# Optimization experiments

Measured on AMD Instinct MI355X. Metric: run time of the kernel, lower is better.

## Reference

```python
import jax, jax.numpy as jnp
import numpy as np

K = 16            # neighbors
QUERY_CHUNK = 256 # SE is applied per chunk of this many query points (matches torch loop)
EPS = 1e-5        # BatchNorm eps (eval mode, running stats)


def bn(x, g, b, m, v):
    # eval-mode batchnorm over last axis (channel-last layout here)
    return (x - m) * (g / jnp.sqrt(v + EPS)) + b


def setup_inputs() -> dict:
    key = jax.random.key(0)
    ks = jax.random.split(key, 16)
    B, Cin, N = 4, 128, 4096
    H, Cout = 128, 256
    se_h = Cout // 4
    r = lambda k, s, sc=1.0: jax.random.normal(k, s, jnp.float32) * sc
    return dict(
        x=r(ks[0], (B, Cin, N)),
        W_edge=r(ks[1], (H, 2 * Cin), 0.05),          # edge_mlp conv2d 1x1
        bn1_g=jnp.ones((H,), jnp.float32), bn1_b=jnp.zeros((H,), jnp.float32),
        bn1_m=r(ks[2], (H,), 0.1), bn1_v=jax.random.uniform(ks[3], (H,), jnp.float32) + 0.5,
        w_att=r(ks[4], (H,), 0.1),                     # att_conv (1,H,1,1)
        W_fuse=r(ks[5], (Cout, H), 0.05),              # fuse conv1d
        bn2_g=jnp.ones((Cout,), jnp.float32), bn2_b=jnp.zeros((Cout,), jnp.float32),
        bn2_m=r(ks[6], (Cout,), 0.1), bn2_v=jax.random.uniform(ks[7], (Cout,), jnp.float32) + 0.5,
        fc1_w=r(ks[8], (se_h, Cout), 0.05), fc1_b=jnp.zeros((se_h,), jnp.float32),
        fc2_w=r(ks[9], (Cout, se_h), 0.05), fc2_b=jnp.zeros((Cout,), jnp.float32),
        W_res=r(ks[10], (Cout, Cin), 0.05),            # res_conv conv1d (in!=out)
        bn3_g=jnp.ones((Cout,), jnp.float32), bn3_b=jnp.zeros((Cout,), jnp.float32),
        bn3_m=r(ks[11], (Cout,), 0.1), bn3_v=jax.random.uniform(ks[12], (Cout,), jnp.float32) + 0.5,
    )


def reference(x, W_edge, bn1_g, bn1_b, bn1_m, bn1_v, w_att,
              W_fuse, bn2_g, bn2_b, bn2_m, bn2_v,
              fc1_w, fc1_b, fc2_w, fc2_b,
              W_res, bn3_g, bn3_b, bn3_m, bn3_v):
    B, Cin, N = x.shape
    x_t = jnp.swapaxes(x, 1, 2)  # (B,N,Cin)

    # KNN on features (dynamic=False -> knn on x.transpose); squared euclidean
    # has the same ordering as torch.cdist(p=2).
    sq = jnp.sum(x_t * x_t, axis=-1)                               # (B,N)
    d2 = sq[:, :, None] + sq[:, None, :] - 2.0 * jnp.einsum('bnc,bmc->bnm', x_t, x_t)
    _, idx = jax.lax.top_k(-d2, K)                                  # (B,N,K) smallest dists

    neigh = jax.vmap(lambda p, i: p[i])(x_t, idx)                   # (B,N,K,Cin)
    center = jnp.broadcast_to(x_t[:, :, None, :], neigh.shape)      # (B,N,K,Cin)
    edge = jnp.concatenate([neigh - center, center], axis=-1)       # (B,N,K,2Cin)

    # edge_mlp: 1x1 conv + BN + ReLU
    h = jax.nn.relu(bn(jnp.einsum('bnkc,hc->bnkh', edge, W_edge),
                       bn1_g, bn1_b, bn1_m, bn1_v))                 # (B,N,K,H)

    # attention over neighbors
    att = jax.nn.softmax(jnp.einsum('bnkh,h->bnk', h, w_att), axis=-1)
    agg = jnp.einsum('bnkh,bnk->bnh', h, att)                       # (B,N,H)

    # fuse conv1d + BN + ReLU
    out = jax.nn.relu(bn(jnp.einsum('bnh,oh->bno', agg, W_fuse),
                         bn2_g, bn2_b, bn2_m, bn2_v))               # (B,N,Cout)

    # SE channel attention, applied per query chunk (matches torch loop semantics)
    Cout = out.shape[-1]
    nc = N // QUERY_CHUNK
    oc = out.reshape(B, nc, QUERY_CHUNK, Cout)
    s = oc.mean(axis=2)                                             # (B,nc,Cout)
    s = jax.nn.relu(jnp.einsum('bmc,hc->bmh', s, fc1_w) + fc1_b)
    s = jax.nn.sigmoid(jnp.einsum('bmh,ch->bmc', s, fc2_w) + fc2_b)
    out = (oc * s[:, :, None, :]).reshape(B, N, Cout)

    # residual projection (in_channels != out_channels)
    res = bn(jnp.einsum('bnc,oc->bno', x_t, W_res), bn3_g, bn3_b, bn3_m, bn3_v)
    out = out + res
    return jnp.swapaxes(out, 1, 2)                                  # (B,Cout,N)
```

## Files before the change

### kernel.cpp

```cpp
#include <hip/hip_runtime.h>
#include <cstddef>

typedef __bf16 bf16;
typedef __bf16 bf16x8 __attribute__((ext_vector_type(8)));
typedef float  f32x4  __attribute__((ext_vector_type(4)));
typedef unsigned short u16;
typedef unsigned long long u64;

#define MFMA16x16(a, b, c) __builtin_amdgcn_mfma_f32_16x16x32_bf16((a), (b), (c), 0, 0, 0)

namespace {
constexpr int BB   = 4;
constexpr int CIN  = 128;
constexpr int NPT  = 4096;
constexpr int KNBR = 16;
constexpr int HED  = 128;
constexpr int COUT = 256;
}

__device__ __forceinline__ unsigned int ord_f32(float f) {
  unsigned int b = __float_as_uint(f);
  return b ^ (0x80000000u | (unsigned int)((int)b >> 31));
}
__device__ __forceinline__ u64 mk_key(float d, int m) {
  return ((u64)ord_f32(d) << 32) | (unsigned int)m;
}

__device__ __forceinline__ void sort16(u64* k) {
  #pragma unroll
  for (int sz = 2; sz <= 16; sz <<= 1) {
    #pragma unroll
    for (int st = sz >> 1; st > 0; st >>= 1) {
      #pragma unroll
      for (int i = 0; i < 16; ++i) {
        const int j = i ^ st;
        if (j > i) {
          const bool up = ((i & sz) == 0);
          const u64 a = k[i], c = k[j];
          const bool sw = up ? (a > c) : (a < c);
          k[i] = sw ? c : a;
          k[j] = sw ? a : c;
        }
      }
    }
  }
}

__device__ __forceinline__ void merge16(u64* R, const u64* B) {
  u64 t[16];
  #pragma unroll
  for (int i = 0; i < 16; ++i) {
    const u64 a = R[i], c = B[15 - i];
    t[i] = (a < c) ? a : c;
  }
  #pragma unroll
  for (int st = 8; st > 0; st >>= 1) {
    #pragma unroll
    for (int i = 0; i < 16; ++i) {
      const int j = i ^ st;
      if (j > i) {
        const u64 a = t[i], c = t[j];
        const bool sw = a > c;
        t[i] = sw ? c : a;
        t[j] = sw ? a : c;
      }
    }
  }
  #pragma unroll
  for (int i = 0; i < 16; ++i) R[i] = t[i];
}

__device__ __forceinline__ void shfl_merge16(u64* R, int mask) {
  u64 B[16];
  #pragma unroll
  for (int i = 0; i < 16; ++i) B[i] = __shfl_xor(R[i], mask, 64);
  merge16(R, B);
}

__global__ __launch_bounds__(256) void k_wconv(const float* __restrict__ We,
                                               const float* __restrict__ Wf,
                                               const float* __restrict__ Wr,
                                               bf16* __restrict__ Web,
                                               bf16* __restrict__ Wfb,
                                               bf16* __restrict__ Wrb) {
  const int i = blockIdx.x * 256 + threadIdx.x;
  const int a = i >> 15;
  const int j = i & 32767;
  const float* src = (a == 0) ? We : (a == 1) ? Wf : Wr;
  bf16*        dst = (a == 0) ? Web : (a == 1) ? Wfb : Wrb;
  dst[j] = (bf16)src[j];
}

__global__ __launch_bounds__(256) void k_prep(const float* __restrict__ x,
                                              bf16* __restrict__ xh,
                                              bf16* __restrict__ xl,
                                              float* __restrict__ sq) {
  __shared__ __attribute__((aligned(16))) bf16 th[64][136];
  __shared__ __attribute__((aligned(16))) bf16 tl[64][136];
  __shared__ float sqp[4][64];
  const int tid = threadIdx.x;
  const int b   = blockIdx.x >> 6;
  const int n0  = (blockIdx.x & 63) << 6;
  const int nl  = tid & 63;
  const int cg  = tid >> 6;
  const float* xb = x + (size_t)b * CIN * NPT;
  float acc = 0.f;
  #pragma unroll
  for (int rep = 0; rep < 32; ++rep) {
    const int c = rep * 4 + cg;
    const float v = xb[(size_t)c * NPT + n0 + nl];
    const bf16 h = (bf16)v;
    const bf16 l = (bf16)(v - (float)h);
    acc += v * v;
    th[nl][c] = h;
    tl[nl][c] = l;
  }
  sqp[cg][nl] = acc;
  __syncthreads();
  bf16* xho = xh + ((size_t)b * NPT + n0) * CIN;
  bf16* xlo = xl + ((size_t)b * NPT + n0) * CIN;
  #pragma unroll
  for (int rep = 0; rep < 32; ++rep) {
    const int e = rep * 256 + tid;
    const int r = e >> 7;
    const int c = e & 127;
    xho[(size_t)r * CIN + c] = th[r][c];
    xlo[(size_t)r * CIN + c] = tl[r][c];
  }
  if (tid < 64) {
    sq[b * NPT + n0 + tid] = sqp[0][tid] + sqp[1][tid] + sqp[2][tid] + sqp[3][tid];
  }
}

__global__ __launch_bounds__(256, 2) void k_knn(const bf16* __restrict__ xh,
                                                const bf16* __restrict__ xl,
                                                const float* __restrict__ sq,
                                                int* __restrict__ knn_idx) {
  __shared__ u64 Lk[32][66];
  const int tid  = threadIdx.x;
  const int w    = tid >> 6;
  const int lane = tid & 63;
  const int col  = lane & 15;
  const int quad = lane >> 4;
  const int b    = blockIdx.x >> 7;
  const int q0   = (blockIdx.x & 127) << 5;
  const bf16*  xhb = xh + (size_t)b * NPT * CIN;
  const bf16*  xlb = xl + (size_t)b * NPT * CIN;
  const float* sqb = sq + b * NPT;

  bf16x8 qh[2][4], ql[2][4];
  float sqn[2];
  #pragma unroll
  for (int t = 0; t < 2; ++t) {
    const bf16* qrh = xhb + (size_t)(q0 + t * 16 + col) * CIN + quad * 8;
    const bf16* qrl = xlb + (size_t)(q0 + t * 16 + col) * CIN + quad * 8;
    #pragma unroll
    for (int ks = 0; ks < 4; ++ks) {
      qh[t][ks] = *(const bf16x8*)(qrh + ks * 32);
      ql[t][ks] = *(const bf16x8*)(qrl + ks * 32);
    }
    sqn[t] = sqb[q0 + t * 16 + col];
  }

  u64 R0[16], R1[16];
  #pragma unroll
  for (int i = 0; i < 16; ++i) { R0[i] = ~0ull; R1[i] = ~0ull; }

  const int cbase = w << 10;
  for (int mt = 0; mt < 16; ++mt) {
    const int m0 = cbase + (mt << 6);
    u64 k0[16], k1[16];
    #pragma unroll
    for (int cb = 0; cb < 4; ++cb) {
      const bf16* crh = xhb + (size_t)(m0 + cb * 16 + col) * CIN + quad * 8;
      const bf16* crl = xlb + (size_t)(m0 + cb * 16 + col) * CIN + quad * 8;
      f32x4 a0 = {0.f, 0.f, 0.f, 0.f};
      f32x4 a1 = {0.f, 0.f, 0.f, 0.f};
      #pragma unroll
      for (int ks = 0; ks < 4; ++ks) {
        const bf16x8 ch_ = *(const bf16x8*)(crh + ks * 32);
        const bf16x8 cl_ = *(const bf16x8*)(crl + ks * 32);
        a0 = MFMA16x16(cl_, qh[0][ks], a0);
        a0 = MFMA16x16(ch_, ql[0][ks], a0);
        a0 = MFMA16x16(ch_, qh[0][ks], a0);
        a1 = MFMA16x16(cl_, qh[1][ks], a1);
        a1 = MFMA16x16(ch_, ql[1][ks], a1);
        a1 = MFMA16x16(ch_, qh[1][ks], a1);
      }
      const f32x4 sqm = *(const f32x4*)(sqb + m0 + cb * 16 + quad * 4);
      #pragma unroll
      for (int r = 0; r < 4; ++r) {
        const int m = m0 + cb * 16 + quad * 4 + r;
        k0[cb * 4 + r] = mk_key((sqn[0] + sqm[r]) - 2.0f * a0[r], m);
        k1[cb * 4 + r] = mk_key((sqn[1] + sqm[r]) - 2.0f * a1[r], m);
      }
    }
    sort16(k0); merge16(R0, k0);
    sort16(k1); merge16(R1, k1);
  }

  shfl_merge16(R0, 16);
  shfl_merge16(R0, 32);
  shfl_merge16(R1, 16);
  shfl_merge16(R1, 32);

  if (quad == 0) {
    #pragma unroll
    for (int i = 0; i < 16; ++i) {
      Lk[col][w * 16 + i]        = R0[i];
      Lk[16 | col][w * 16 + i]   = R1[i];
    }
  }
  __syncthreads();

  if (tid < 64) {
    const int q = tid >> 1;
    const int j = tid & 1;
    u64 A[16], Bv[16];
    #pragma unroll
    for (int i = 0; i < 16; ++i) {
      A[i]  = Lk[q][(2 * j) * 16 + i];
      Bv[i] = Lk[q][(2 * j + 1) * 16 + i];
    }
    merge16(A, Bv);
    #pragma unroll
    for (int i = 0; i < 16; ++i) Lk[q][j * 16 + i] = A[i];
  }
  __syncthreads();
  if (tid < 32) {
    u64 A[16], Bv[16];
    #pragma unroll
    for (int i = 0; i < 16; ++i) {
      A[i]  = Lk[tid][i];
      Bv[i] = Lk[tid][16 + i];
    }
    merge16(A, Bv);
    int* op = knn_idx + (size_t)(b * NPT + q0 + tid) * KNBR;
    #pragma unroll
    for (int i = 0; i < 16; ++i) op[i] = (int)(A[i] & 0xFFFFFFFFull);
  }
}

__global__ __launch_bounds__(256) void k_edge(const bf16* __restrict__ xh,
                                              const bf16* __restrict__ xl,
                                              const int* __restrict__ knn_idx,
                                              const bf16* __restrict__ We,
                                              const float* __restrict__ g1, const float* __restrict__ b1,
                                              const float* __restrict__ m1, const float* __restrict__ v1,
                                              const float* __restrict__ watt,
                                              bf16* __restrict__ agg) {
  __shared__ __attribute__((aligned(16))) bf16 Ew[4][16][264];
  __shared__ float s1[HED], t1[HED], wat[HED];
  const int tid  = threadIdx.x;
  const int w    = tid >> 6;
  const int lane = tid & 63;
  const int col  = lane & 15;
  const int quad = lane >> 4;
  if (tid < HED) {
    const float ss = g1[tid] / sqrtf(v1[tid] + 1e-5f);
    s1[tid] = ss;
    t1[tid] = b1[tid] - m1[tid] * ss;
    wat[tid] = watt[tid];
  }
  __syncthreads();
  const int gw = blockIdx.x * 4 + w;
  for (int it = 0; it < 4; ++it) {
    const int p = gw * 4 + it;
    const int b = p >> 12;
    const int n = p & 4095;
    const bf16* xhb = xh + (size_t)b * NPT * CIN;
    const bf16* xlb = xl + (size_t)b * NPT * CIN;
    const int my = knn_idx[(size_t)p * KNBR + col];
    const int m  = __shfl(my, lane >> 2);
    const int sub = lane & 3;
    const int kn  = lane >> 2;
    const bf16* nh = xhb + (size_t)m * CIN + sub * 32;
    const bf16* nl_ = xlb + (size_t)m * CIN + sub * 32;
    const bf16* ch = xhb + (size_t)n * CIN + sub * 32;
    const bf16* cl = xlb + (size_t)n * CIN + sub * 32;
    #pragma unroll
    for (int j = 0; j < 4; ++j) {
      const bf16x8 nhv = *(const bf16x8*)(nh + j * 8);
      const bf16x8 nlv = *(const bf16x8*)(nl_ + j * 8);
      const bf16x8 chv = *(const bf16x8*)(ch + j * 8);
      const bf16x8 clv = *(const bf16x8*)(cl + j * 8);
      bf16x8 dv, cv;
      #pragma unroll
      for (int e = 0; e < 8; ++e) {
        const float nf = (float)nhv[e] + (float)nlv[e];
        const float cf = (float)chv[e] + (float)clv[e];
        dv[e] = (bf16)(nf - cf);
        cv[e] = (bf16)cf;
      }
      *(bf16x8*)&Ew[w][kn][sub * 32 + j * 8]       = dv;
      *(bf16x8*)&Ew[w][kn][128 + sub * 32 + j * 8] = cv;
    }
    __syncthreads();
    const f32x4 zero4 = {0.f, 0.f, 0.f, 0.f};
    f32x4 acc[8];
    #pragma unroll
    for (int hb = 0; hb < 8; ++hb) acc[hb] = zero4;
    #pragma unroll
    for (int ks = 0; ks < 8; ++ks) {
      const bf16x8 af = *(const bf16x8*)&Ew[w][col][ks * 32 + quad * 8];
      #pragma unroll
      for (int hb = 0; hb < 8; ++hb) {
        const bf16x8 bfv = *(const bf16x8*)(We + (size_t)(hb * 16 + col) * 256 + ks * 32 + quad * 8);
        acc[hb] = MFMA16x16(af, bfv, acc[hb]);
      }
    }
    float h[8][4];
    float lg[4] = {0.f, 0.f, 0.f, 0.f};
    #pragma unroll
    for (int hb = 0; hb < 8; ++hb) {
      const int hc = hb * 16 + col;
      const float ss = s1[hc], tt = t1[hc], ww = wat[hc];
      #pragma unroll
      for (int r = 0; r < 4; ++r) {
        const float hv = fmaxf(acc[hb][r] * ss + tt, 0.f);
        h[hb][r] = hv;
        lg[r] += hv * ww;
      }
    }
    #pragma unroll
    for (int r = 0; r < 4; ++r) {
      float vv = lg[r];
      vv += __shfl_xor(vv, 1);
      vv += __shfl_xor(vv, 2);
      vv += __shfl_xor(vv, 4);
      vv += __shfl_xor(vv, 8);
      lg[r] = vv;
    }
    float mx = fmaxf(fmaxf(lg[0], lg[1]), fmaxf(lg[2], lg[3]));
    mx = fmaxf(mx, __shfl_xor(mx, 16));
    mx = fmaxf(mx, __shfl_xor(mx, 32));
    float ex[4];
    float sm = 0.f;
    #pragma unroll
    for (int r = 0; r < 4; ++r) { ex[r] = expf(lg[r] - mx); sm += ex[r]; }
    sm += __shfl_xor(sm, 16);
    sm += __shfl_xor(sm, 32);
    const float inv = 1.0f / sm;
    float ag[8];
    #pragma unroll
    for (int hb = 0; hb < 8; ++hb) {
      float a = h[hb][0] * ex[0] + h[hb][1] * ex[1] + h[hb][2] * ex[2] + h[hb][3] * ex[3];
      a += __shfl_xor(a, 16);
      a += __shfl_xor(a, 32);
      ag[hb] = a * inv;
    }
    if (quad == 0) {
      bf16* ao = agg + (size_t)p * HED;
      #pragma unroll
      for (int hb = 0; hb < 8; ++hb) ao[hb * 16 + col] = (bf16)ag[hb];
    }
    __syncthreads();
  }
}

__global__ __launch_bounds__(256) void k_fuse(const bf16* __restrict__ agg,
                                              const bf16* __restrict__ Wf,
                                              const float* __restrict__ g2, const float* __restrict__ b2,
                                              const float* __restrict__ m2, const float* __restrict__ v2,
                                              bf16* __restrict__ outp) {
  const int tid  = threadIdx.x;
  const int w    = tid >> 6;
  const int lane = tid & 63;
  const int col  = lane & 15;
  const int quad = lane >> 4;
  const int p0   = (blockIdx.x * 4 + w) * 16;
  bf16x8 afr[4];
  const bf16* arow = agg + (size_t)(p0 + col) * HED + quad * 8;
  #pragma unroll
  for (int ks = 0; ks < 4; ++ks) afr[ks] = *(const bf16x8*)(arow + ks * 32);
  #pragma unroll
  for (int ob = 0; ob < 16; ++ob) {
    f32x4 acc = {0.f, 0.f, 0.f, 0.f};
    const bf16* brow = Wf + (size_t)(ob * 16 + col) * HED + quad * 8;
    #pragma unroll
    for (int ks = 0; ks < 4; ++ks)
      acc = MFMA16x16(afr[ks], *(const bf16x8*)(brow + ks * 32), acc);
    const int o = ob * 16 + col;
    const float ss = g2[o] / sqrtf(v2[o] + 1e-5f);
    const float tt = b2[o] - m2[o] * ss;
    #pragma unroll
    for (int r = 0; r < 4; ++r) {
      outp[(size_t)(p0 + quad * 4 + r) * COUT + o] = (bf16)fmaxf(acc[r] * ss + tt, 0.f);
    }
  }
}

__global__ __launch_bounds__(256) void k_se(const bf16* __restrict__ outp,
                                            const float* __restrict__ f1w, const float* __restrict__ f1b,
                                            const float* __restrict__ f2w, const float* __restrict__ f2b,
                                            float* __restrict__ sse) {
  __shared__ float mean_s[COUT];
  __shared__ float h1[64];
  const int bc  = blockIdx.x;
  const int tid = threadIdx.x;
  const bf16* base = outp + (size_t)bc * 256 * COUT;
  float s = 0.f;
  for (int p2 = 0; p2 < 256; ++p2) s += (float)base[(size_t)p2 * COUT + tid];
  mean_s[tid] = s * (1.0f / 256.0f);
  __syncthreads();
  if (tid < 64) {
    float a = f1b[tid];
    for (int c = 0; c < COUT; ++c) a += f1w[tid * COUT + c] * mean_s[c];
    h1[tid] = fmaxf(a, 0.f);
  }
  __syncthreads();
  float a = f2b[tid];
  #pragma unroll
  for (int j = 0; j < 64; ++j) a += f2w[tid * 64 + j] * h1[j];
  sse[(size_t)bc * COUT + tid] = 1.0f / (1.0f + expf(-a));
}

__global__ __launch_bounds__(256) void k_final(const bf16* __restrict__ xh,
                                               const bf16* __restrict__ Wr,
                                               const float* __restrict__ g3, const float* __restrict__ b3,
                                               const float* __restrict__ m3, const float* __restrict__ v3,
                                               const bf16* __restrict__ outp,
                                               const float* __restrict__ sse,
                                               float* __restrict__ out) {
  const int tid  = threadIdx.x;
  const int w    = tid >> 6;
  const int lane = tid & 63;
  const int col  = lane & 15;
  const int quad = lane >> 4;
  const int p0   = (blockIdx.x * 4 + w) * 16;
  const int b    = p0 >> 12;
  const int n0l  = p0 & 4095;
  bf16x8 afr[4];
  const bf16* arow = xh + (size_t)(p0 + col) * CIN + quad * 8;
  #pragma unroll
  for (int ks = 0; ks < 4; ++ks) afr[ks] = *(const bf16x8*)(arow + ks * 32);
  const float* scb = sse + (size_t)(b * 16 + (n0l >> 8)) * COUT;
  #pragma unroll
  for (int ob = 0; ob < 16; ++ob) {
    f32x4 acc = {0.f, 0.f, 0.f, 0.f};
    const bf16* brow = Wr + (size_t)(ob * 16 + col) * CIN + quad * 8;
    #pragma unroll
    for (int ks = 0; ks < 4; ++ks)
      acc = MFMA16x16(afr[ks], *(const bf16x8*)(brow + ks * 32), acc);
    const int o = ob * 16 + col;
    const float ss = g3[o] / sqrtf(v3[o] + 1e-5f);
    const float tt = b3[o] - m3[o] * ss;
    const float sc = scb[o];
    f32x4 pk;
    #pragma unroll
    for (int r = 0; r < 4; ++r) {
      const float res = acc[r] * ss + tt;
      pk[r] = (float)outp[(size_t)(p0 + quad * 4 + r) * COUT + o] * sc + res;
    }
    float* op = out + (size_t)(b * COUT + o) * NPT + n0l + quad * 4;
    *(f32x4*)op = pk;
  }
}

extern "C" void kernel_launch(void* const* d_in, const int* in_sizes, int n_in,
                              void* d_out, int out_size, void* d_ws, size_t ws_size,
                              hipStream_t stream) {
  (void)in_sizes; (void)n_in; (void)out_size; (void)ws_size;
  const float* x    = (const float*)d_in[0];
  const float* We   = (const float*)d_in[1];
  const float* g1   = (const float*)d_in[2];
  const float* b1   = (const float*)d_in[3];
  const float* m1   = (const float*)d_in[4];
  const float* v1   = (const float*)d_in[5];
  const float* watt = (const float*)d_in[6];
  const float* Wf   = (const float*)d_in[7];
  const float* g2   = (const float*)d_in[8];
  const float* b2   = (const float*)d_in[9];
  const float* m2   = (const float*)d_in[10];
  const float* v2   = (const float*)d_in[11];
  const float* f1w  = (const float*)d_in[12];
  const float* f1b  = (const float*)d_in[13];
  const float* f2w  = (const float*)d_in[14];
  const float* f2b  = (const float*)d_in[15];
  const float* Wr   = (const float*)d_in[16];
  const float* g3   = (const float*)d_in[17];
  const float* b3   = (const float*)d_in[18];
  const float* m3   = (const float*)d_in[19];
  const float* v3   = (const float*)d_in[20];

  char* ws = (char*)d_ws;
  size_t off = 0;
  bf16*  xth  = (bf16*)(ws + off);  off += (size_t)BB * NPT * CIN * 2;
  bf16*  xtl  = (bf16*)(ws + off);  off += (size_t)BB * NPT * CIN * 2;
  float* sq   = (float*)(ws + off); off += (size_t)BB * NPT * 4;
  int*   idxp = (int*)(ws + off);   off += (size_t)BB * NPT * KNBR * 4;
  bf16*  aggp = (bf16*)(ws + off);  off += (size_t)BB * NPT * HED * 2;
  bf16*  outp = (bf16*)(ws + off);  off += (size_t)BB * NPT * COUT * 2;
  float* ssep = (float*)(ws + off); off += (size_t)BB * 16 * COUT * 4;
  bf16*  Web  = (bf16*)(ws + off);  off += (size_t)HED * 2 * CIN * 2;
  bf16*  Wfb  = (bf16*)(ws + off);  off += (size_t)COUT * HED * 2;
  bf16*  Wrb  = (bf16*)(ws + off);  off += (size_t)COUT * CIN * 2;

  float* out = (float*)d_out;

  k_wconv<<<384, 256, 0, stream>>>(We, Wf, Wr, Web, Wfb, Wrb);
  k_prep<<<256, 256, 0, stream>>>(x, xth, xtl, sq);
  k_knn<<<512, 256, 0, stream>>>(xth, xtl, sq, idxp);
  k_edge<<<1024, 256, 0, stream>>>(xth, xtl, idxp, Web, g1, b1, m1, v1, watt, aggp);
  k_fuse<<<256, 256, 0, stream>>>(aggp, Wfb, g2, b2, m2, v2, outp);
  k_se<<<64, 256, 0, stream>>>(outp, f1w, f1b, f2w, f2b, ssep);
  k_final<<<256, 256, 0, stream>>>(xth, Wrb, g3, b3, m3, v3, outp, ssep, out);
}
```

Before: 434.3 us.

## Two-pass KNN: float-only top-k threshold, then recompute and collect candidates

Measured after the change: 513.5 us. 18.2% more time.

```diff
diff --git a/kernel.cpp b/kernel.cpp
--- a/kernel.cpp
+++ b/kernel.cpp
@@ -70,11 +70,51 @@
   for (int i = 0; i < 16; ++i) R[i] = t[i];
 }
 
-__device__ __forceinline__ void shfl_merge16(u64* R, int mask) {
-  u64 B[16];
+__device__ __forceinline__ void fsort16(float* k) {
+  #pragma unroll
+  for (int sz = 2; sz <= 16; sz <<= 1) {
+    #pragma unroll
+    for (int st = sz >> 1; st > 0; st >>= 1) {
+      #pragma unroll
+      for (int i = 0; i < 16; ++i) {
+        const int j = i ^ st;
+        if (j > i) {
+          const bool up = ((i & sz) == 0);
+          const float a = k[i], c = k[j];
+          const float lo = fminf(a, c), hi = fmaxf(a, c);
+          k[i] = up ? lo : hi;
+          k[j] = up ? hi : lo;
+        }
+      }
+    }
+  }
+}
+
+__device__ __forceinline__ void fmerge16(float* R, const float* B) {
+  float t[16];
+  #pragma unroll
+  for (int i = 0; i < 16; ++i) t[i] = fminf(R[i], B[15 - i]);
+  #pragma unroll
+  for (int st = 8; st > 0; st >>= 1) {
+    #pragma unroll
+    for (int i = 0; i < 16; ++i) {
+      const int j = i ^ st;
+      if (j > i) {
+        const float a = t[i], c = t[j];
+        t[i] = fminf(a, c);
+        t[j] = fmaxf(a, c);
+      }
+    }
+  }
+  #pragma unroll
+  for (int i = 0; i < 16; ++i) R[i] = t[i];
+}
+
+__device__ __forceinline__ void fshfl_merge16(float* R, int mask) {
+  float B[16];
   #pragma unroll
   for (int i = 0; i < 16; ++i) B[i] = __shfl_xor(R[i], mask, 64);
-  merge16(R, B);
+  fmerge16(R, B);
 }
 
 __global__ __launch_bounds__(256) void k_wconv(const float* __restrict__ We,
@@ -136,7 +176,10 @@
                                                 const bf16* __restrict__ xl,
                                                 const float* __restrict__ sq,
                                                 int* __restrict__ knn_idx) {
-  __shared__ u64 Lk[32][66];
+  __shared__ float Lf[32][66];
+  __shared__ float Thr[32];
+  __shared__ unsigned int cnt[32];
+  __shared__ u64 buf[32][32];
   const int tid  = threadIdx.x;
   const int w    = tid >> 6;
   const int lane = tid & 63;
@@ -162,14 +205,18 @@
     sqn[t] = sqb[q0 + t * 16 + col];
   }
 
-  u64 R0[16], R1[16];
-  #pragma unroll
-  for (int i = 0; i < 16; ++i) { R0[i] = ~0ull; R1[i] = ~0ull; }
+  float R0[16], R1[16];
+  #pragma unroll
+  for (int i = 0; i < 16; ++i) {
+    R0[i] = __builtin_inff();
+    R1[i] = __builtin_inff();
+  }
 
   const int cbase = w << 10;
+
   for (int mt = 0; mt < 16; ++mt) {
     const int m0 = cbase + (mt << 6);
-    u64 k0[16], k1[16];
+    float k0v[16], k1v[16];
     #pragma unroll
     for (int cb = 0; cb < 4; ++cb) {
       const bf16* crh = xhb + (size_t)(m0 + cb * 16 + col) * CIN + quad * 8;
@@ -190,25 +237,26 @@
       const f32x4 sqm = *(const f32x4*)(sqb + m0 + cb * 16 + quad * 4);
       #pragma unroll
       for (int r = 0; r < 4; ++r) {
-        const int m = m0 + cb * 16 + quad * 4 + r;
-        k0[cb * 4 + r] = mk_key((sqn[0] + sqm[r]) - 2.0f * a0[r], m);
-        k1[cb * 4 + r] = mk_key((sqn[1] + sqm[r]) - 2.0f * a1[r], m);
-      }
-    }
-    sort16(k0); merge16(R0, k0);
-    sort16(k1); merge16(R1, k1);
-  }
-
-  shfl_merge16(R0, 16);
-  shfl_merge16(R0, 32);
-  shfl_merge16(R1, 16);
-  shfl_merge16(R1, 32);
+        const float s0 = sqn[0] + sqm[r];
+        const float s1 = sqn[1] + sqm[r];
+        k0v[cb * 4 + r] = fmaf(-2.0f, a0[r], s0);
+        k1v[cb * 4 + r] = fmaf(-2.0f, a1[r], s1);
+      }
+    }
+    fsort16(k0v); fmerge16(R0, k0v);
+    fsort16(k1v); fmerge16(R1, k1v);
+  }
+
+  fshfl_merge16(R0, 16);
+  fshfl_merge16(R0, 32);
+  fshfl_merge16(R1, 16);
+  fshfl_merge16(R1, 32);
 
   if (quad == 0) {
     #pragma unroll
     for (int i = 0; i < 16; ++i) {
-      Lk[col][w * 16 + i]        = R0[i];
-      Lk[16 | col][w * 16 + i]   = R1[i];
+      Lf[col][w * 16 + i]      = R0[i];
+      Lf[16 | col][w * 16 + i] = R1[i];
     }
   }
   __syncthreads();
@@ -216,23 +264,98 @@
   if (tid < 64) {
     const int q = tid >> 1;
     const int j = tid & 1;
-    u64 A[16], Bv[16];
+    float A[16], Bv[16];
     #pragma unroll
     for (int i = 0; i < 16; ++i) {
-      A[i]  = Lk[q][(2 * j) * 16 + i];
-      Bv[i] = Lk[q][(2 * j + 1) * 16 + i];
-    }
-    merge16(A, Bv);
-    #pragma unroll
-    for (int i = 0; i < 16; ++i) Lk[q][j * 16 + i] = A[i];
+      A[i]  = Lf[q][(2 * j) * 16 + i];
+      Bv[i] = Lf[q][(2 * j + 1) * 16 + i];
+    }
+    fmerge16(A, Bv);
+    #pragma unroll
+    for (int i = 0; i < 16; ++i) Lf[q][j * 16 + i] = A[i];
+  }
+  __syncthreads();
+  if (tid < 32) {
+    float A[16], Bv[16];
+    #pragma unroll
+    for (int i = 0; i < 16; ++i) {
+      A[i]  = Lf[tid][i];
+      Bv[i] = Lf[tid][16 + i];
+    }
+    fmerge16(A, Bv);
+    Thr[tid] = A[15];
+    cnt[tid] = 0;
+  }
+  __syncthreads();
+
+  const float thr0 = Thr[col];
+  const float thr1 = Thr[16 | col];
+
+  for (int mt = 0; mt < 16; ++mt) {
+    const int m0 = cbase + (mt << 6);
+    #pragma unroll
+    for (int cb = 0; cb < 4; ++cb) {
+      const bf16* crh = xhb + (size_t)(m0 + cb * 16 + col) * CIN + quad * 8;
+      const bf16* crl = xlb + (size_t)(m0 + cb * 16 + col) * CIN + quad * 8;
+      f32x4 a0 = {0.f, 0.f, 0.f, 0.f};
+      f32x4 a1 = {0.f, 0.f, 0.f, 0.f};
+      #pragma unroll
+      for (int ks = 0; ks < 4; ++ks) {
+        const bf16x8 ch_ = *(const bf16x8*)(crh + ks * 32);
+        const bf16x8 cl_ = *(const bf16x8*)(crl + ks * 32);
+        a0 = MFMA16x16(cl_, qh[0][ks], a0);
+        a0 = MFMA16x16(ch_, ql[0][ks], a0);
+        a0 = MFMA16x16(ch_, qh[0][ks], a0);
+        a1 = MFMA16x16(cl_, qh[1][ks], a1);
+        a1 = MFMA16x16(ch_, ql[1][ks], a1);
+        a1 = MFMA16x16(ch_, qh[1][ks], a1);
+      }
+      const f32x4 sqm = *(const f32x4*)(sqb + m0 + cb * 16 + quad * 4);
+      #pragma unroll
+      for (int r = 0; r < 4; ++r) {
+        const int m = m0 + cb * 16 + quad * 4 + r;
+        const float s0 = sqn[0] + sqm[r];
+        const float s1 = sqn[1] + sqm[r];
+        const float d0 = fmaf(-2.0f, a0[r], s0);
+        const float d1 = fmaf(-2.0f, a1[r], s1);
+        const bool h0 = (d0 <= thr0);
+        const bool h1 = (d1 <= thr1);
+        if (h0 | h1) {
+          if (h0) {
+            const unsigned pos = atomicAdd(&cnt[col], 1u);
+            if (pos < 32) buf[col][pos] = mk_key(d0, m);
+          }
+          if (h1) {
+            const unsigned pos = atomicAdd(&cnt[16 | col], 1u);
+            if (pos < 32) buf[16 | col][pos] = mk_key(d1, m);
+          }
+        }
+      }
+    }
+  }
+  __syncthreads();
+
+  if (tid < 64) {
+    const int q = tid >> 1;
+    const int h = tid & 1;
+    const unsigned n = cnt[q] < 32u ? cnt[q] : 32u;
+    u64 A[16];
+    #pragma unroll
+    for (int i = 0; i < 16; ++i) {
+      const unsigned p = h * 16 + i;
+      A[i] = (p < n) ? buf[q][p] : ~0ull;
+    }
+    sort16(A);
+    #pragma unroll
+    for (int i = 0; i < 16; ++i) buf[q][h * 16 + i] = A[i];
   }
   __syncthreads();
   if (tid < 32) {
     u64 A[16], Bv[16];
     #pragma unroll
     for (int i = 0; i < 16; ++i) {
-      A[i]  = Lk[tid][i];
-      Bv[i] = Lk[tid][16 + i];
+      A[i]  = buf[tid][i];
+      Bv[i] = buf[tid][16 + i];
     }
     merge16(A, Bv);
     int* op = knn_idx + (size_t)(b * NPT + q0 + tid) * KNBR;
```
